# Kernel optimization log

Measured on AMD Instinct MI355X. Metric: run time of the kernel, lower is better.

The kernel has to match this reference:

```python
import jax, jax.numpy as jnp
import numpy as np

N, E, F_IN, HID, HEADS, NT, B = 50000, 400000, 32, 64, 4, 20, 64
IN1 = F_IN + HID  # 96, conv1 input dim after concat with node-type embedding


def _glorot(key, shape):
    fan_in = shape[0]
    return jax.random.normal(key, shape, dtype=jnp.float32) / np.sqrt(fan_in)


def setup_inputs() -> dict:
    key = jax.random.key(0)
    ks = jax.random.split(key, 40)
    inp = {
        "x": jax.random.normal(ks[0], (N, F_IN), dtype=jnp.float32),
        "edge_index": jax.random.randint(ks[1], (2, E), 0, N, dtype=jnp.int32),
        "edge_attr": jax.random.normal(ks[2], (E,), dtype=jnp.float32),
        "batch": jnp.sort(jax.random.randint(ks[3], (N,), 0, B, dtype=jnp.int32)),
        "node_type": jax.random.randint(ks[4], (N,), 0, NT, dtype=jnp.int32),
        # parameters
        "node_emb": jax.random.normal(ks[5], (NT, HID), dtype=jnp.float32) * 0.1,
        "edge_W": _glorot(ks[6], (1, HID)), "edge_b": jnp.zeros((HID,), jnp.float32),
        # GATConv 1 (in=96, out=64, heads=4, edge_dim=64, concat=False)
        "W1": _glorot(ks[7], (IN1, HEADS * HID)),
        "att_src1": jax.random.normal(ks[8], (HEADS, HID), jnp.float32) * 0.1,
        "att_dst1": jax.random.normal(ks[9], (HEADS, HID), jnp.float32) * 0.1,
        "We1": _glorot(ks[10], (HID, HEADS * HID)),
        "att_e1": jax.random.normal(ks[11], (HEADS, HID), jnp.float32) * 0.1,
        "b1": jnp.zeros((HID,), jnp.float32),
        # GATConv 2 (in=64)
        "W2": _glorot(ks[12], (HID, HEADS * HID)),
        "att_src2": jax.random.normal(ks[13], (HEADS, HID), jnp.float32) * 0.1,
        "att_dst2": jax.random.normal(ks[14], (HEADS, HID), jnp.float32) * 0.1,
        "We2": _glorot(ks[15], (HID, HEADS * HID)),
        "att_e2": jax.random.normal(ks[16], (HEADS, HID), jnp.float32) * 0.1,
        "b2": jnp.zeros((HID,), jnp.float32),
        # SAGEConv (mean aggr): out = mean_agg @ Wl + x @ Wr + b
        "sage_Wl": _glorot(ks[17], (HID, HID)), "sage_Wr": _glorot(ks[18], (HID, HID)),
        "sage_b": jnp.zeros((HID,), jnp.float32),
        "lin1_W": _glorot(ks[19], (HID, HID)), "lin1_b": jnp.zeros((HID,), jnp.float32),
        "lin2_W": _glorot(ks[20], (HID, HID)), "lin2_b": jnp.zeros((HID,), jnp.float32),
        "tel_W": _glorot(ks[21], (HID, 1)), "tel_b": jnp.zeros((1,), jnp.float32),
        "comp_W": _glorot(ks[22], (HID, 1)), "comp_b": jnp.zeros((1,), jnp.float32),
        "pch_W": _glorot(ks[23], (HID, 1)), "pch_b": jnp.zeros((1,), jnp.float32),
    }
    return inp


def _gat(x, src, dst, edge_h, W, att_s, att_d, We, att_e, b):
    n = x.shape[0]
    h = (x @ W).reshape(n, HEADS, HID)                       # [N,H,C]
    a_s = (h * att_s).sum(-1)                                # [N,H]
    a_d = (h * att_d).sum(-1)
    e = (edge_h @ We).reshape(-1, HEADS, HID)                # [E,H,C]
    a_e = (e * att_e).sum(-1)                                # [E,H]
    alpha = jax.nn.leaky_relu(a_s[src] + a_d[dst] + a_e, 0.2)
    m = jax.ops.segment_max(alpha, dst, num_segments=n)
    m = jnp.where(jnp.isfinite(m), m, 0.0)
    ex = jnp.exp(alpha - m[dst])
    den = jax.ops.segment_sum(ex, dst, num_segments=n)
    alpha = ex / (den[dst] + 1e-16)                          # segment softmax per dst
    out = jax.ops.segment_sum(h[src] * alpha[..., None], dst, num_segments=n)
    return out.mean(axis=1) + b                              # concat=False -> head mean


def reference(x, edge_index, edge_attr, batch, node_type, node_emb, edge_W, edge_b,
              W1, att_src1, att_dst1, We1, att_e1, b1,
              W2, att_src2, att_dst2, We2, att_e2, b2,
              sage_Wl, sage_Wr, sage_b, lin1_W, lin1_b, lin2_W, lin2_b,
              tel_W, tel_b, comp_W, comp_b, pch_W, pch_b):
    src, dst = edge_index[0], edge_index[1]
    edge_h = edge_attr[:, None] @ edge_W + edge_b            # [E,HID]
    h = jnp.concatenate([x, node_emb[node_type]], axis=-1)   # [N,96]
    h = jax.nn.elu(_gat(h, src, dst, edge_h, W1, att_src1, att_dst1, We1, att_e1, b1))
    h = jax.nn.elu(_gat(h, src, dst, edge_h, W2, att_src2, att_dst2, We2, att_e2, b2))
    # SAGEConv with mean aggregation
    deg = jax.ops.segment_sum(jnp.ones((src.shape[0],), h.dtype), dst, num_segments=N)
    agg = jax.ops.segment_sum(h[src], dst, num_segments=N) / jnp.maximum(deg, 1.0)[:, None]
    h = jax.nn.elu(agg @ sage_Wl + h @ sage_Wr + sage_b)
    # global mean pool over graphs
    cnt = jax.ops.segment_sum(jnp.ones((N,), h.dtype), batch, num_segments=B)
    g = jax.ops.segment_sum(h, batch, num_segments=B) / jnp.maximum(cnt, 1.0)[:, None]
    g = jax.nn.elu(g @ lin1_W + lin1_b)                      # dropout is identity in eval
    g = g @ lin2_W + lin2_b
    return (g @ tel_W + tel_b, g @ comp_W + comp_b, g @ pch_W + pch_b)
```

## Files before the change

### kernel.cpp

```cpp
#include <hip/hip_runtime.h>
#include <hip/hip_bf16.h>


#define NN 50000
#define NE 400000
#define FIN 32
#define NBATCH 64

typedef __hip_bfloat16 bf16;
typedef short bf16x8 __attribute__((ext_vector_type(8)));
typedef float f32x4 __attribute__((ext_vector_type(4)));

__device__ __forceinline__ float b2f(bf16 v) { return __bfloat162float(v); }
__device__ __forceinline__ float lrelu(float x) { return x > 0.f ? x : 0.2f * x; }
__device__ __forceinline__ float eluf(float x) { return x > 0.f ? x : (expf(x) - 1.f); }

__device__ __forceinline__ float4 f4fma(float s, float4 w, float4 c) {
  c.x = fmaf(s, w.x, c.x); c.y = fmaf(s, w.y, c.y);
  c.z = fmaf(s, w.z, c.z); c.w = fmaf(s, w.w, c.w);
  return c;
}

__device__ __forceinline__ float4 upk4(uint2 u) {
  float4 f;
  f.x = __uint_as_float(u.x << 16);
  f.y = __uint_as_float(u.x & 0xffff0000u);
  f.z = __uint_as_float(u.y << 16);
  f.w = __uint_as_float(u.y & 0xffff0000u);
  return f;
}

__device__ __forceinline__ unsigned short bfbits(float f) {
  bf16 b = __float2bfloat16(f);
  unsigned short u;
  __builtin_memcpy(&u, &b, 2);
  return u;
}
__device__ __forceinline__ float hi_f(unsigned short u) {
  return __uint_as_float((unsigned int)u << 16);
}

__global__ __launch_bounds__(256) void k_pq(
    const float* __restrict__ We1, const float* __restrict__ atte1,
    const float* __restrict__ We2, const float* __restrict__ atte2,
    const float* __restrict__ edgeW, const float* __restrict__ edgeB,
    float* __restrict__ pq) {
  int t = threadIdx.x, h = t >> 6, c = t & 63;
  float sW1 = 0.f, sB1 = 0.f, sW2 = 0.f, sB2 = 0.f;
  for (int j = 0; j < 64; ++j) {
    float w = edgeW[j], b = edgeB[j];
    float we1 = We1[j * 256 + h * 64 + c];
    float we2 = We2[j * 256 + h * 64 + c];
    sW1 += w * we1; sB1 += b * we1;
    sW2 += w * we2; sB2 += b * we2;
  }
  float a1 = atte1[h * 64 + c], a2 = atte2[h * 64 + c];
  float p1 = sW1 * a1, q1 = sB1 * a1, p2 = sW2 * a2, q2 = sB2 * a2;
  for (int o = 32; o; o >>= 1) {
    p1 += __shfl_xor(p1, o); q1 += __shfl_xor(q1, o);
    p2 += __shfl_xor(p2, o); q2 += __shfl_xor(q2, o);
  }
  if (c == 0) { pq[h] = p1; pq[4 + h] = q1; pq[8 + h] = p2; pq[12 + h] = q2; }
}

__global__ void k_hist(const int* __restrict__ dst, int* __restrict__ cnt) {
  int e = blockIdx.x * 256 + threadIdx.x;
  if (e < NE) atomicAdd(&cnt[dst[e]], 1);
}

__global__ __launch_bounds__(1024) void k_scan(const int* __restrict__ cnt,
                                               int* __restrict__ off) {
  __shared__ int wsum[16];
  __shared__ int carry;
  int t = threadIdx.x, lane = t & 63, w = t >> 6;
  if (t == 0) { carry = 0; off[0] = 0; }
  __syncthreads();
  for (int base = 0; base < NN; base += 1024) {
    int idx = base + t;
    int v = (idx < NN) ? cnt[idx] : 0;
    int s = v;
    for (int o = 1; o < 64; o <<= 1) { int u = __shfl_up(s, o); if (lane >= o) s += u; }
    if (lane == 63) wsum[w] = s;
    __syncthreads();
    if (t < 16) {
      int ws = wsum[t];
      for (int o = 1; o < 16; o <<= 1) { int u = __shfl_up(ws, o); if (t >= o) ws += u; }
      wsum[t] = ws;
    }
    __syncthreads();
    int add = carry + (w ? wsum[w - 1] : 0);
    if (idx < NN) off[idx + 1] = add + s;
    __syncthreads();
    if (t == 0) carry += wsum[15];
    __syncthreads();
  }
}

__global__ void k_scatter(const int* __restrict__ src, const int* __restrict__ dst,
                          const float* __restrict__ ea, const int* __restrict__ off,
                          int* __restrict__ cur, int* __restrict__ csr_src,
                          float* __restrict__ csr_ea) {
  int e = blockIdx.x * 256 + threadIdx.x;
  if (e >= NE) return;
  int d = dst[e];
  int slot = off[d] + atomicAdd(&cur[d], 1);
  csr_src[slot] = src[e];
  csr_ea[slot] = ea[e];
}

__global__ __launch_bounds__(256) void k_splitA(
    const float* __restrict__ x, const int* __restrict__ ntype,
    const float* __restrict__ emb, unsigned short* __restrict__ Ah,
    unsigned short* __restrict__ Al) {
  const int total = NN * 96;
  for (int i = blockIdx.x * 256 + threadIdx.x; i < total; i += gridDim.x * 256) {
    int n = i / 96, k = i - n * 96;
    float v = (k < FIN) ? x[n * FIN + k] : emb[ntype[n] * 64 + (k - FIN)];
    unsigned short h = bfbits(v);
    Ah[i] = h;
    Al[i] = bfbits(v - hi_f(h));
  }
}

__global__ __launch_bounds__(256) void k_splitW(
    const float* __restrict__ W1, const float* __restrict__ W2,
    unsigned short* __restrict__ B1h, unsigned short* __restrict__ B1l,
    unsigned short* __restrict__ B2h, unsigned short* __restrict__ B2l) {
  int t = blockIdx.x * 256 + threadIdx.x;
  if (t < 256 * 96) {
    int n = t / 96, k = t - n * 96;
    float v = W1[k * 256 + n];
    unsigned short h = bfbits(v);
    B1h[t] = h; B1l[t] = bfbits(v - hi_f(h));
  }
  if (t < 256 * 64) {
    int n = t >> 6, k = t & 63;
    float v = W2[k * 256 + n];
    unsigned short h = bfbits(v);
    B2h[t] = h; B2l[t] = bfbits(v - hi_f(h));
  }
}

template <int K>
__global__ __launch_bounds__(256) void k_mm_mfma(
    const unsigned short* __restrict__ Ah, const unsigned short* __restrict__ Al,
    const unsigned short* __restrict__ Bh, const unsigned short* __restrict__ Bl,
    const float* __restrict__ atts, const float* __restrict__ attd,
    bf16* __restrict__ hmat, float* __restrict__ as_, float* __restrict__ ad_) {
  int m0 = blockIdx.x * 64;
  int w = threadIdx.x >> 6;
  int lane = threadIdx.x & 63;
  int lr = lane & 15;
  int lc = lane >> 4;
  float attsv[4], attdv[4];
  #pragma unroll
  for (int nt = 0; nt < 4; ++nt) {
    attsv[nt] = atts[w * 64 + nt * 16 + lr];
    attdv[nt] = attd[w * 64 + nt * 16 + lr];
  }
  f32x4 acc[4][4] = {};
  #pragma unroll
  for (int ks = 0; ks < K; ks += 32) {
    int koff = ks + lc * 8;
    bf16x8 ah[4], al[4], bh[4], bl[4];
    #pragma unroll
    for (int mt = 0; mt < 4; ++mt) {
      int m = m0 + mt * 16 + lr;
      if (m > NN - 1) m = NN - 1;
      ah[mt] = *reinterpret_cast<const bf16x8*>(&Ah[(size_t)m * K + koff]);
      al[mt] = *reinterpret_cast<const bf16x8*>(&Al[(size_t)m * K + koff]);
    }
    #pragma unroll
    for (int nt = 0; nt < 4; ++nt) {
      int n = w * 64 + nt * 16 + lr;
      bh[nt] = *reinterpret_cast<const bf16x8*>(&Bh[(size_t)n * K + koff]);
      bl[nt] = *reinterpret_cast<const bf16x8*>(&Bl[(size_t)n * K + koff]);
    }
    #pragma unroll
    for (int mt = 0; mt < 4; ++mt) {
      #pragma unroll
      for (int nt = 0; nt < 4; ++nt) {
        acc[mt][nt] = __builtin_amdgcn_mfma_f32_16x16x32_bf16(ah[mt], bh[nt], acc[mt][nt], 0, 0, 0);
        acc[mt][nt] = __builtin_amdgcn_mfma_f32_16x16x32_bf16(al[mt], bh[nt], acc[mt][nt], 0, 0, 0);
        acc[mt][nt] = __builtin_amdgcn_mfma_f32_16x16x32_bf16(ah[mt], bl[nt], acc[mt][nt], 0, 0, 0);
      }
    }
  }
  #pragma unroll
  for (int mt = 0; mt < 4; ++mt) {
    #pragma unroll
    for (int reg = 0; reg < 4; ++reg) {
      int row = m0 + mt * 16 + lc * 4 + reg;
      float sS = 0.f, sD = 0.f;
      #pragma unroll
      for (int nt = 0; nt < 4; ++nt) {
        float v = acc[mt][nt][reg];
        sS += v * attsv[nt];
        sD += v * attdv[nt];
      }
      for (int o = 1; o < 16; o <<= 1) {
        sS += __shfl_xor(sS, o);
        sD += __shfl_xor(sD, o);
      }
      if (row < NN) {
        #pragma unroll
        for (int nt = 0; nt < 4; ++nt)
          hmat[(size_t)row * 256 + w * 64 + nt * 16 + lr] =
              __float2bfloat16(acc[mt][nt][reg]);
        if (lr == 0) { as_[row * 4 + w] = sS; ad_[row * 4 + w] = sD; }
      }
    }
  }
}

__global__ __launch_bounds__(256) void k_gat(
    const int* __restrict__ off, const int* __restrict__ csr_src,
    const float* __restrict__ csr_ea, const float* __restrict__ as_,
    const float* __restrict__ ad_, const float* __restrict__ pq, int pqo,
    const bf16* __restrict__ hmat, const float* __restrict__ bias,
    float* __restrict__ outf, unsigned short* __restrict__ oph,
    unsigned short* __restrict__ opl) {
  __shared__ float wlds[4][256];
  int wv = threadIdx.x >> 6;
  int wid = (blockIdx.x << 2) + wv;
  int lane = threadIdx.x & 63;
  if (wid >= NN) return;
  int beg = off[wid], end = off[wid + 1];
  int deg = end - beg;
  int hsel = lane >> 4;
  float4 D = reinterpret_cast<const float4*>(ad_)[wid];
  float p0 = pq[pqo + 0], p1 = pq[pqo + 1], p2 = pq[pqo + 2], p3 = pq[pqo + 3];
  float q0 = pq[pqo + 4], q1 = pq[pqo + 5], q2 = pq[pqo + 6], q3 = pq[pqo + 7];
  float4 acc = {0.f, 0.f, 0.f, 0.f};

  if (deg <= 64) {
    bool valid = lane < deg;
    float lx = -INFINITY, ly = -INFINITY, lz = -INFINITY, lw = -INFINITY;
    if (valid) {
      int s = csr_src[beg + lane];
      float ea = csr_ea[beg + lane];
      float4 A = reinterpret_cast<const float4*>(as_)[s];
      lx = lrelu(A.x + D.x + ea * p0 + q0);
      ly = lrelu(A.y + D.y + ea * p1 + q1);
      lz = lrelu(A.z + D.z + ea * p2 + q2);
      lw = lrelu(A.w + D.w + ea * p3 + q3);
    }
    float m0 = lx, m1 = ly, m2 = lz, m3 = lw;
    for (int o = 32; o; o >>= 1) {
      m0 = fmaxf(m0, __shfl_xor(m0, o));
      m1 = fmaxf(m1, __shfl_xor(m1, o));
      m2 = fmaxf(m2, __shfl_xor(m2, o));
      m3 = fmaxf(m3, __shfl_xor(m3, o));
    }
    float w0 = valid ? __expf(lx - m0) : 0.f;
    float w1 = valid ? __expf(ly - m1) : 0.f;
    float w2 = valid ? __expf(lz - m2) : 0.f;
    float w3 = valid ? __expf(lw - m3) : 0.f;
    float s0 = w0, s1 = w1, s2 = w2, s3 = w3;
    for (int o = 32; o; o >>= 1) {
      s0 += __shfl_xor(s0, o); s1 += __shfl_xor(s1, o);
      s2 += __shfl_xor(s2, o); s3 += __shfl_xor(s3, o);
    }
    float4 wv4;
    wv4.x = w0 / (s0 + 1e-16f);
    wv4.y = w1 / (s1 + 1e-16f);
    wv4.z = w2 / (s2 + 1e-16f);
    wv4.w = w3 / (s3 + 1e-16f);
    reinterpret_cast<float4*>(&wlds[wv][0])[lane] = wv4;
    const float* wp = &wlds[wv][0];
    int j = 0;
    for (; j + 4 <= deg; j += 4) {
      int sA = csr_src[beg + j + 0];
      int sB = csr_src[beg + j + 1];
      int sC = csr_src[beg + j + 2];
      int sD = csr_src[beg + j + 3];
      float wA = wp[4 * (j + 0) + hsel];
      float wB = wp[4 * (j + 1) + hsel];
      float wC = wp[4 * (j + 2) + hsel];
      float wD = wp[4 * (j + 3) + hsel];
      uint2 uA = *reinterpret_cast<const uint2*>(&hmat[(size_t)sA * 256 + 4 * lane]);
      uint2 uB = *reinterpret_cast<const uint2*>(&hmat[(size_t)sB * 256 + 4 * lane]);
      uint2 uC = *reinterpret_cast<const uint2*>(&hmat[(size_t)sC * 256 + 4 * lane]);
      uint2 uD = *reinterpret_cast<const uint2*>(&hmat[(size_t)sD * 256 + 4 * lane]);
      acc = f4fma(wA, upk4(uA), acc);
      acc = f4fma(wB, upk4(uB), acc);
      acc = f4fma(wC, upk4(uC), acc);
      acc = f4fma(wD, upk4(uD), acc);
    }
    for (; j < deg; ++j) {
      int s = csr_src[beg + j];
      float w = wp[4 * j + hsel];
      uint2 u = *reinterpret_cast<const uint2*>(&hmat[(size_t)s * 256 + 4 * lane]);
      acc = f4fma(w, upk4(u), acc);
    }
  } else {
    float m0 = -INFINITY, m1 = -INFINITY, m2 = -INFINITY, m3 = -INFINITY;
    float s0 = 0.f, s1 = 0.f, s2 = 0.f, s3 = 0.f;
    for (int e = beg + lane; e < end; e += 64) {
      int s = csr_src[e];
      float ea = csr_ea[e];
      float4 A = reinterpret_cast<const float4*>(as_)[s];
      float lx = lrelu(A.x + D.x + ea * p0 + q0);
      float ly = lrelu(A.y + D.y + ea * p1 + q1);
      float lz = lrelu(A.z + D.z + ea * p2 + q2);
      float lw = lrelu(A.w + D.w + ea * p3 + q3);
      float nm;
      nm = fmaxf(m0, lx); s0 = s0 * __expf(m0 - nm) + __expf(lx - nm); m0 = nm;
      nm = fmaxf(m1, ly); s1 = s1 * __expf(m1 - nm) + __expf(ly - nm); m1 = nm;
      nm = fmaxf(m2, lz); s2 = s2 * __expf(m2 - nm) + __expf(lz - nm); m2 = nm;
      nm = fmaxf(m3, lw); s3 = s3 * __expf(m3 - nm) + __expf(lw - nm); m3 = nm;
    }
    for (int o = 32; o; o >>= 1) {
      float om, os, nm;
      om = __shfl_xor(m0, o); os = __shfl_xor(s0, o); nm = fmaxf(m0, om);
      s0 = s0 * __expf(fmaxf(m0 - nm, -80.f)) + os * __expf(fmaxf(om - nm, -80.f)); m0 = nm;
      om = __shfl_xor(m1, o); os = __shfl_xor(s1, o); nm = fmaxf(m1, om);
      s1 = s1 * __expf(fmaxf(m1 - nm, -80.f)) + os * __expf(fmaxf(om - nm, -80.f)); m1 = nm;
      om = __shfl_xor(m2, o); os = __shfl_xor(s2, o); nm = fmaxf(m2, om);
      s2 = s2 * __expf(fmaxf(m2 - nm, -80.f)) + os * __expf(fmaxf(om - nm, -80.f)); m2 = nm;
      om = __shfl_xor(m3, o); os = __shfl_xor(s3, o); nm = fmaxf(m3, om);
      s3 = s3 * __expf(fmaxf(m3 - nm, -80.f)) + os * __expf(fmaxf(om - nm, -80.f)); m3 = nm;
    }
    float i0 = 1.f / (s0 + 1e-16f), i1 = 1.f / (s1 + 1e-16f);
    float i2 = 1.f / (s2 + 1e-16f), i3 = 1.f / (s3 + 1e-16f);
    float Dh = hsel == 0 ? D.x : hsel == 1 ? D.y : hsel == 2 ? D.z : D.w;
    float ph = hsel == 0 ? p0 : hsel == 1 ? p1 : hsel == 2 ? p2 : p3;
    float qh = hsel == 0 ? q0 : hsel == 1 ? q1 : hsel == 2 ? q2 : q3;
    float mh = hsel == 0 ? m0 : hsel == 1 ? m1 : hsel == 2 ? m2 : m3;
    float ih = hsel == 0 ? i0 : hsel == 1 ? i1 : hsel == 2 ? i2 : i3;
    for (int j = beg; j < end; ++j) {
      int s = csr_src[j];
      float ea = csr_ea[j];
      float4 A = reinterpret_cast<const float4*>(as_)[s];
      float Ah = hsel == 0 ? A.x : hsel == 1 ? A.y : hsel == 2 ? A.z : A.w;
      float l = lrelu(Ah + Dh + ea * ph + qh);
      float w = __expf(l - mh) * ih;
      uint2 u = *reinterpret_cast<const uint2*>(&hmat[(size_t)s * 256 + 4 * lane]);
      acc = f4fma(w, upk4(u), acc);
    }
  }
  acc.x += __shfl_xor(acc.x, 16); acc.y += __shfl_xor(acc.y, 16);
  acc.z += __shfl_xor(acc.z, 16); acc.w += __shfl_xor(acc.w, 16);
  acc.x += __shfl_xor(acc.x, 32); acc.y += __shfl_xor(acc.y, 32);
  acc.z += __shfl_xor(acc.z, 32); acc.w += __shfl_xor(acc.w, 32);
  if (lane < 16) {
    float4 bv = reinterpret_cast<const float4*>(bias)[lane];
    float4 r;
    r.x = eluf(0.25f * acc.x + bv.x);
    r.y = eluf(0.25f * acc.y + bv.y);
    r.z = eluf(0.25f * acc.z + bv.z);
    r.w = eluf(0.25f * acc.w + bv.w);
    if (outf) reinterpret_cast<float4*>(&outf[(size_t)wid * 64])[lane] = r;
    if (oph) {
      ushort4 h4, l4;
      h4.x = bfbits(r.x); l4.x = bfbits(r.x - hi_f(h4.x));
      h4.y = bfbits(r.y); l4.y = bfbits(r.y - hi_f(h4.y));
      h4.z = bfbits(r.z); l4.z = bfbits(r.z - hi_f(h4.z));
      h4.w = bfbits(r.w); l4.w = bfbits(r.w - hi_f(h4.w));
      *reinterpret_cast<ushort4*>(&oph[(size_t)wid * 64 + lane * 4]) = h4;
      *reinterpret_cast<ushort4*>(&opl[(size_t)wid * 64 + lane * 4]) = l4;
    }
  }
}

__global__ __launch_bounds__(256) void k_agg(
    const int* __restrict__ off, const int* __restrict__ csr_src,
    const float* __restrict__ h3, float* __restrict__ agg) {
  int wid = (blockIdx.x << 2) + (threadIdx.x >> 6);
  int lane = threadIdx.x & 63;
  if (wid >= NN) return;
  int beg = off[wid], end = off[wid + 1];
  float acc = 0.f;
  int e = beg;
  for (; e + 4 <= end; e += 4) {
    int s0 = csr_src[e + 0], s1 = csr_src[e + 1];
    int s2 = csr_src[e + 2], s3 = csr_src[e + 3];
    float v0 = h3[(size_t)s0 * 64 + lane];
    float v1 = h3[(size_t)s1 * 64 + lane];
    float v2 = h3[(size_t)s2 * 64 + lane];
    float v3 = h3[(size_t)s3 * 64 + lane];
    acc += (v0 + v1) + (v2 + v3);
  }
  for (; e < end; ++e) acc += h3[(size_t)csr_src[e] * 64 + lane];
  agg[(size_t)wid * 64 + lane] = acc / fmaxf((float)(end - beg), 1.f);
}

__global__ __launch_bounds__(256) void k_sage_mm(
    const float* __restrict__ agg, const float* __restrict__ h3,
    const float* __restrict__ Wl, const float* __restrict__ Wr,
    const float* __restrict__ bias, float* __restrict__ out) {
  __shared__ float WlS[4096];
  __shared__ float WrS[4096];
  __shared__ float Ag[2048];
  __shared__ float Hr[2048];
  int t = threadIdx.x;
  for (int i = t; i < 4096; i += 256) { WlS[i] = Wl[i]; WrS[i] = Wr[i]; }
  int ct = t & 15, rg = t >> 4;
  float4 bv = reinterpret_cast<const float4*>(bias)[ct];
  for (int r0 = blockIdx.x * 32; r0 < NN; r0 += gridDim.x * 32) {
    for (int i = t; i < 2048; i += 256) {
      int n = r0 + (i >> 6);
      float va = 0.f, vh = 0.f;
      if (n < NN) {
        va = agg[(size_t)n * 64 + (i & 63)];
        vh = h3[(size_t)n * 64 + (i & 63)];
      }
      Ag[i] = va; Hr[i] = vh;
    }
    __syncthreads();
    float4 c0 = {0.f, 0.f, 0.f, 0.f}, c1 = c0;
    const float* a0 = &Ag[(rg * 2 + 0) * 64];
    const float* a1 = &Ag[(rg * 2 + 1) * 64];
    const float* h0 = &Hr[(rg * 2 + 0) * 64];
    const float* h1 = &Hr[(rg * 2 + 1) * 64];
    #pragma unroll 4
    for (int k = 0; k < 64; k += 4) {
      float4 wl0 = *reinterpret_cast<const float4*>(&WlS[(k + 0) * 64 + ct * 4]);
      float4 wl1 = *reinterpret_cast<const float4*>(&WlS[(k + 1) * 64 + ct * 4]);
      float4 wl2 = *reinterpret_cast<const float4*>(&WlS[(k + 2) * 64 + ct * 4]);
      float4 wl3 = *reinterpret_cast<const float4*>(&WlS[(k + 3) * 64 + ct * 4]);
      float4 wr0 = *reinterpret_cast<const float4*>(&WrS[(k + 0) * 64 + ct * 4]);
      float4 wr1 = *reinterpret_cast<const float4*>(&WrS[(k + 1) * 64 + ct * 4]);
      float4 wr2 = *reinterpret_cast<const float4*>(&WrS[(k + 2) * 64 + ct * 4]);
      float4 wr3 = *reinterpret_cast<const float4*>(&WrS[(k + 3) * 64 + ct * 4]);
      float4 aa0 = *reinterpret_cast<const float4*>(&a0[k]);
      float4 aa1 = *reinterpret_cast<const float4*>(&a1[k]);
      float4 hh0 = *reinterpret_cast<const float4*>(&h0[k]);
      float4 hh1 = *reinterpret_cast<const float4*>(&h1[k]);
      c0 = f4fma(aa0.x, wl0, c0); c0 = f4fma(aa0.y, wl1, c0);
      c0 = f4fma(aa0.z, wl2, c0); c0 = f4fma(aa0.w, wl3, c0);
      c0 = f4fma(hh0.x, wr0, c0); c0 = f4fma(hh0.y, wr1, c0);
      c0 = f4fma(hh0.z, wr2, c0); c0 = f4fma(hh0.w, wr3, c0);
      c1 = f4fma(aa1.x, wl0, c1); c1 = f4fma(aa1.y, wl1, c1);
      c1 = f4fma(aa1.z, wl2, c1); c1 = f4fma(aa1.w, wl3, c1);
      c1 = f4fma(hh1.x, wr0, c1); c1 = f4fma(hh1.y, wr1, c1);
      c1 = f4fma(hh1.z, wr2, c1); c1 = f4fma(hh1.w, wr3, c1);
    }
    int n0 = r0 + rg * 2;
    if (n0 + 0 < NN) {
      float4 r;
      r.x = eluf(c0.x + bv.x); r.y = eluf(c0.y + bv.y);
      r.z = eluf(c0.z + bv.z); r.w = eluf(c0.w + bv.w);
      *reinterpret_cast<float4*>(&out[(size_t)(n0 + 0) * 64 + ct * 4]) = r;
    }
    if (n0 + 1 < NN) {
      float4 r;
      r.x = eluf(c1.x + bv.x); r.y = eluf(c1.y + bv.y);
      r.z = eluf(c1.z + bv.z); r.w = eluf(c1.w + bv.w);
      *reinterpret_cast<float4*>(&out[(size_t)(n0 + 1) * 64 + ct * 4]) = r;
    }
    __syncthreads();
  }
}

__global__ __launch_bounds__(256) void k_pool2(const float* __restrict__ hs,
                                               const int* __restrict__ batch,
                                               float* __restrict__ g) {
  int cid = (blockIdx.x << 2) + (threadIdx.x >> 6);
  int lane = threadIdx.x & 63;
  int n0 = cid * 32;
  if (n0 >= NN) return;
  int n1 = n0 + 32 < NN ? n0 + 32 : NN;
  int cur = batch[n0];
  float acc = 0.f;
  for (int n = n0; n < n1; ++n) {
    int b = batch[n];
    if (b != cur) {
      atomicAdd(&g[cur * 64 + lane], acc);
      acc = 0.f;
      cur = b;
    }
    acc += hs[(size_t)n * 64 + lane];
  }
  atomicAdd(&g[cur * 64 + lane], acc);
}

__device__ __forceinline__ int lowerb(const int* __restrict__ a, int n, int key) {
  int lo = 0, hi = n;
  while (lo < hi) { int mid = (lo + hi) >> 1; if (a[mid] < key) lo = mid + 1; else hi = mid; }
  return lo;
}

__global__ __launch_bounds__(256) void k_head(
    const float* __restrict__ g, const int* __restrict__ batch,
    const float* __restrict__ l1W, const float* __restrict__ l1b,
    const float* __restrict__ l2W, const float* __restrict__ l2b,
    const float* __restrict__ telW, const float* __restrict__ telb,
    const float* __restrict__ compW, const float* __restrict__ compb,
    const float* __restrict__ pchW, const float* __restrict__ pchb,
    float* __restrict__ out) {
  __shared__ float gS[4096];
  __shared__ float WS[4096];
  __shared__ float hS[4096];
  __shared__ float invc[64];
  int t = threadIdx.x;
  if (t < 64) {
    int lo = lowerb(batch, NN, t), hi = lowerb(batch, NN, t + 1);
    invc[t] = 1.f / fmaxf((float)(hi - lo), 1.f);
  }
  for (int i = t; i < 4096; i += 256) WS[i] = l1W[i];
  __syncthreads();
  for (int i = t; i < 4096; i += 256) gS[i] = g[i] * invc[i >> 6];
  __syncthreads();
  for (int i = t; i < 4096; i += 256) {
    int r = i >> 6, j = i & 63;
    float s = 0.f;
    for (int k = 0; k < 64; ++k) s += gS[r * 64 + k] * WS[k * 64 + j];
    hS[i] = eluf(s + l1b[j]);
  }
  __syncthreads();
  for (int i = t; i < 4096; i += 256) WS[i] = l2W[i];
  __syncthreads();
  for (int i = t; i < 4096; i += 256) {
    int r = i >> 6, j = i & 63;
    float s = 0.f;
    for (int k = 0; k < 64; ++k) s += hS[r * 64 + k] * WS[k * 64 + j];
    gS[i] = s + l2b[j];
  }
  __syncthreads();
  if (t < 192) {
    int head = t >> 6, r = t & 63;
    const float* Wv = head == 0 ? telW : (head == 1 ? compW : pchW);
    float bb = head == 0 ? telb[0] : (head == 1 ? compb[0] : pchb[0]);
    float s = 0.f;
    for (int k = 0; k < 64; ++k) s += gS[r * 64 + k] * Wv[k];
    out[t] = s + bb;
  }
}

extern "C" void kernel_launch(void* const* d_in, const int* in_sizes, int n_in,
                              void* d_out, int out_size, void* d_ws, size_t ws_size,
                              hipStream_t stream) {
  const float* x     = (const float*)d_in[0];
  const int*   eidx  = (const int*)d_in[1];
  const float* eattr = (const float*)d_in[2];
  const int*   batch = (const int*)d_in[3];
  const int*   ntype = (const int*)d_in[4];
  const float* nemb  = (const float*)d_in[5];
  const float* edgeW = (const float*)d_in[6];
  const float* edgeB = (const float*)d_in[7];
  const float* W1    = (const float*)d_in[8];
  const float* atts1 = (const float*)d_in[9];
  const float* attd1 = (const float*)d_in[10];
  const float* We1   = (const float*)d_in[11];
  const float* atte1 = (const float*)d_in[12];
  const float* b1    = (const float*)d_in[13];
  const float* W2    = (const float*)d_in[14];
  const float* atts2 = (const float*)d_in[15];
  const float* attd2 = (const float*)d_in[16];
  const float* We2   = (const float*)d_in[17];
  const float* atte2 = (const float*)d_in[18];
  const float* b2    = (const float*)d_in[19];
  const float* sageWl = (const float*)d_in[20];
  const float* sageWr = (const float*)d_in[21];
  const float* sageB  = (const float*)d_in[22];
  const float* l1W = (const float*)d_in[23];
  const float* l1b = (const float*)d_in[24];
  const float* l2W = (const float*)d_in[25];
  const float* l2b = (const float*)d_in[26];
  const float* telW  = (const float*)d_in[27];
  const float* telb  = (const float*)d_in[28];
  const float* compW = (const float*)d_in[29];
  const float* compb = (const float*)d_in[30];
  const float* pchW  = (const float*)d_in[31];
  const float* pchb  = (const float*)d_in[32];

  char* wp = (char*)d_ws;
  auto alloc = [&](size_t bytes) -> char* {
    char* p = wp;
    wp += (bytes + 255) & ~(size_t)255;
    return p;
  };
  float*  pq      = (float*)alloc(16 * 4);
  int*    cnt     = (int*)alloc((size_t)NN * 4);
  int*    off     = (int*)alloc(((size_t)NN + 1) * 4);
  int*    csr_src = (int*)alloc((size_t)NE * 4);
  float*  csr_ea  = (float*)alloc((size_t)NE * 4);
  float*  as_     = (float*)alloc((size_t)NN * 16);
  float*  ad_     = (float*)alloc((size_t)NN * 16);
  bf16*   hmat    = (bf16*)alloc((size_t)NN * 256 * 2);
  float*  nodeB   = (float*)alloc((size_t)NN * 64 * 4);
  float*  aggbuf  = (float*)alloc((size_t)NN * 64 * 4);
  unsigned short* B1h = (unsigned short*)alloc(256 * 96 * 2);
  unsigned short* B1l = (unsigned short*)alloc(256 * 96 * 2);
  unsigned short* B2h = (unsigned short*)alloc(256 * 64 * 2);
  unsigned short* B2l = (unsigned short*)alloc(256 * 64 * 2);
  char* R = alloc((size_t)NN * 96 * 2 * 2);
  unsigned short* A1h = (unsigned short*)R;
  unsigned short* A1l = A1h + (size_t)NN * 96;
  unsigned short* A2h = (unsigned short*)R;
  unsigned short* A2l = A2h + (size_t)NN * 64;
  float* sageout = (float*)R;
  float* gbuf = (float*)alloc(64 * 64 * 4);

  const int* srcI = eidx;
  const int* dstI = eidx + NE;

  hipMemsetAsync(cnt, 0, (size_t)NN * 4, stream);
  hipMemsetAsync(gbuf, 0, 64 * 64 * 4, stream);
  k_pq<<<1, 256, 0, stream>>>(We1, atte1, We2, atte2, edgeW, edgeB, pq);
  k_hist<<<(NE + 255) / 256, 256, 0, stream>>>(dstI, cnt);
  k_scan<<<1, 1024, 0, stream>>>(cnt, off);
  hipMemsetAsync(cnt, 0, (size_t)NN * 4, stream);
  k_scatter<<<(NE + 255) / 256, 256, 0, stream>>>(srcI, dstI, eattr, off, cnt,
                                                  csr_src, csr_ea);
  k_splitW<<<96, 256, 0, stream>>>(W1, W2, B1h, B1l, B2h, B2l);
  k_splitA<<<2048, 256, 0, stream>>>(x, ntype, nemb, A1h, A1l);
  k_mm_mfma<96><<<(NN + 63) / 64, 256, 0, stream>>>(
      A1h, A1l, B1h, B1l, atts1, attd1, hmat, as_, ad_);
  k_gat<<<NN / 4, 256, 0, stream>>>(off, csr_src, csr_ea, as_, ad_, pq, 0,
                                    hmat, b1, nullptr, A2h, A2l);
  k_mm_mfma<64><<<(NN + 63) / 64, 256, 0, stream>>>(
      A2h, A2l, B2h, B2l, atts2, attd2, hmat, as_, ad_);
  k_gat<<<NN / 4, 256, 0, stream>>>(off, csr_src, csr_ea, as_, ad_, pq, 8,
                                    hmat, b2, nodeB, nullptr, nullptr);
  k_agg<<<NN / 4, 256, 0, stream>>>(off, csr_src, nodeB, aggbuf);
  k_sage_mm<<<1024, 256, 0, stream>>>(aggbuf, nodeB, sageWl, sageWr, sageB,
                                      sageout);
  k_pool2<<<((NN + 31) / 32 + 3) / 4, 256, 0, stream>>>(sageout, batch, gbuf);
  k_head<<<1, 256, 0, stream>>>(gbuf, batch, l1W, l1b, l2W, l2b, telW, telb,
                                compW, compb, pchW, pchb, (float*)d_out);
}
```

Before: 468.2 us.

## Widen GAT/SAGE gathers to 128-bit loads with multi-edge lanes; merge prep kernels

In the low-degree GAT path, each half-wave now gathers a different neighbor row using 16-byte loads, with 8 features per lane, and the halves are then reduced with cross-lane shuffles. The SAGE mean-aggregation kernel likewise has four lane groups each loading a different neighbor's row as float4, reduced with shuffles at the end. The weight-split kernel is merged into the pq kernel, and the scatter now counts down the histogram with atomicSub, which removes a memset. These changes aim to raise memory-level parallelism, cut load instructions and drop launches, at the cost of extra shuffle reductions and lanes idling on ragged tails.

```diff
diff --git a/kernel.cpp b/kernel.cpp
--- a/kernel.cpp
+++ b/kernel.cpp
@@ -30,6 +30,15 @@
   return f;
 }
 
+__device__ __forceinline__ float4 upk4u(unsigned int lo, unsigned int hi) {
+  float4 f;
+  f.x = __uint_as_float(lo << 16);
+  f.y = __uint_as_float(lo & 0xffff0000u);
+  f.z = __uint_as_float(hi << 16);
+  f.w = __uint_as_float(hi & 0xffff0000u);
+  return f;
+}
+
 __device__ __forceinline__ unsigned short bfbits(float f) {
   bf16 b = __float2bfloat16(f);
   unsigned short u;
@@ -40,27 +49,46 @@
   return __uint_as_float((unsigned int)u << 16);
 }
 
-__global__ __launch_bounds__(256) void k_pq(
+__global__ __launch_bounds__(256) void k_prep(
+    const float* __restrict__ W1, const float* __restrict__ W2,
     const float* __restrict__ We1, const float* __restrict__ atte1,
     const float* __restrict__ We2, const float* __restrict__ atte2,
     const float* __restrict__ edgeW, const float* __restrict__ edgeB,
+    unsigned short* __restrict__ B1h, unsigned short* __restrict__ B1l,
+    unsigned short* __restrict__ B2h, unsigned short* __restrict__ B2l,
     float* __restrict__ pq) {
-  int t = threadIdx.x, h = t >> 6, c = t & 63;
-  float sW1 = 0.f, sB1 = 0.f, sW2 = 0.f, sB2 = 0.f;
-  for (int j = 0; j < 64; ++j) {
-    float w = edgeW[j], b = edgeB[j];
-    float we1 = We1[j * 256 + h * 64 + c];
-    float we2 = We2[j * 256 + h * 64 + c];
-    sW1 += w * we1; sB1 += b * we1;
-    sW2 += w * we2; sB2 += b * we2;
-  }
-  float a1 = atte1[h * 64 + c], a2 = atte2[h * 64 + c];
-  float p1 = sW1 * a1, q1 = sB1 * a1, p2 = sW2 * a2, q2 = sB2 * a2;
-  for (int o = 32; o; o >>= 1) {
-    p1 += __shfl_xor(p1, o); q1 += __shfl_xor(q1, o);
-    p2 += __shfl_xor(p2, o); q2 += __shfl_xor(q2, o);
-  }
-  if (c == 0) { pq[h] = p1; pq[4 + h] = q1; pq[8 + h] = p2; pq[12 + h] = q2; }
+  if (blockIdx.x == 96) {
+    int t = threadIdx.x, h = t >> 6, c = t & 63;
+    float sW1 = 0.f, sB1 = 0.f, sW2 = 0.f, sB2 = 0.f;
+    for (int j = 0; j < 64; ++j) {
+      float w = edgeW[j], b = edgeB[j];
+      float we1 = We1[j * 256 + h * 64 + c];
+      float we2 = We2[j * 256 + h * 64 + c];
+      sW1 += w * we1; sB1 += b * we1;
+      sW2 += w * we2; sB2 += b * we2;
+    }
+    float a1 = atte1[h * 64 + c], a2 = atte2[h * 64 + c];
+    float p1 = sW1 * a1, q1 = sB1 * a1, p2 = sW2 * a2, q2 = sB2 * a2;
+    for (int o = 32; o; o >>= 1) {
+      p1 += __shfl_xor(p1, o); q1 += __shfl_xor(q1, o);
+      p2 += __shfl_xor(p2, o); q2 += __shfl_xor(q2, o);
+    }
+    if (c == 0) { pq[h] = p1; pq[4 + h] = q1; pq[8 + h] = p2; pq[12 + h] = q2; }
+    return;
+  }
+  int t = blockIdx.x * 256 + threadIdx.x;
+  if (t < 256 * 96) {
+    int n = t / 96, k = t - n * 96;
+    float v = W1[k * 256 + n];
+    unsigned short h = bfbits(v);
+    B1h[t] = h; B1l[t] = bfbits(v - hi_f(h));
+  }
+  if (t < 256 * 64) {
+    int n = t >> 6, k = t & 63;
+    float v = W2[k * 256 + n];
+    unsigned short h = bfbits(v);
+    B2h[t] = h; B2l[t] = bfbits(v - hi_f(h));
+  }
 }
 
 __global__ void k_hist(const int* __restrict__ dst, int* __restrict__ cnt) {
@@ -98,12 +126,13 @@
 
 __global__ void k_scatter(const int* __restrict__ src, const int* __restrict__ dst,
                           const float* __restrict__ ea, const int* __restrict__ off,
-                          int* __restrict__ cur, int* __restrict__ csr_src,
+                          int* __restrict__ cnt, int* __restrict__ csr_src,
                           float* __restrict__ csr_ea) {
   int e = blockIdx.x * 256 + threadIdx.x;
   if (e >= NE) return;
   int d = dst[e];
-  int slot = off[d] + atomicAdd(&cur[d], 1);
+  int r = atomicSub(&cnt[d], 1);
+  int slot = off[d] + r - 1;
   csr_src[slot] = src[e];
   csr_ea[slot] = ea[e];
 }
@@ -119,25 +148,6 @@
     unsigned short h = bfbits(v);
     Ah[i] = h;
     Al[i] = bfbits(v - hi_f(h));
-  }
-}
-
-__global__ __launch_bounds__(256) void k_splitW(
-    const float* __restrict__ W1, const float* __restrict__ W2,
-    unsigned short* __restrict__ B1h, unsigned short* __restrict__ B1l,
-    unsigned short* __restrict__ B2h, unsigned short* __restrict__ B2l) {
-  int t = blockIdx.x * 256 + threadIdx.x;
-  if (t < 256 * 96) {
-    int n = t / 96, k = t - n * 96;
-    float v = W1[k * 256 + n];
-    unsigned short h = bfbits(v);
-    B1h[t] = h; B1l[t] = bfbits(v - hi_f(h));
-  }
-  if (t < 256 * 64) {
-    int n = t >> 6, k = t & 63;
-    float v = W2[k * 256 + n];
-    unsigned short h = bfbits(v);
-    B2h[t] = h; B2l[t] = bfbits(v - hi_f(h));
   }
 }
 
@@ -227,11 +237,9 @@
   if (wid >= NN) return;
   int beg = off[wid], end = off[wid + 1];
   int deg = end - beg;
-  int hsel = lane >> 4;
   float4 D = reinterpret_cast<const float4*>(ad_)[wid];
   float p0 = pq[pqo + 0], p1 = pq[pqo + 1], p2 = pq[pqo + 2], p3 = pq[pqo + 3];
   float q0 = pq[pqo + 4], q1 = pq[pqo + 5], q2 = pq[pqo + 6], q3 = pq[pqo + 7];
-  float4 acc = {0.f, 0.f, 0.f, 0.f};
 
   if (deg <= 64) {
     bool valid = lane < deg;
@@ -268,32 +276,71 @@
     wv4.w = w3 / (s3 + 1e-16f);
     reinterpret_cast<float4*>(&wlds[wv][0])[lane] = wv4;
     const float* wp = &wlds[wv][0];
+    int g = lane >> 5;
+    int c5 = lane & 31;
+    int hsl = c5 >> 3;
+    float4 aA = {0.f, 0.f, 0.f, 0.f}, aB = aA;
     int j = 0;
-    for (; j + 4 <= deg; j += 4) {
-      int sA = csr_src[beg + j + 0];
-      int sB = csr_src[beg + j + 1];
-      int sC = csr_src[beg + j + 2];
-      int sD = csr_src[beg + j + 3];
-      float wA = wp[4 * (j + 0) + hsel];
-      float wB = wp[4 * (j + 1) + hsel];
-      float wC = wp[4 * (j + 2) + hsel];
-      float wD = wp[4 * (j + 3) + hsel];
-      uint2 uA = *reinterpret_cast<const uint2*>(&hmat[(size_t)sA * 256 + 4 * lane]);
-      uint2 uB = *reinterpret_cast<const uint2*>(&hmat[(size_t)sB * 256 + 4 * lane]);
-      uint2 uC = *reinterpret_cast<const uint2*>(&hmat[(size_t)sC * 256 + 4 * lane]);
-      uint2 uD = *reinterpret_cast<const uint2*>(&hmat[(size_t)sD * 256 + 4 * lane]);
-      acc = f4fma(wA, upk4(uA), acc);
-      acc = f4fma(wB, upk4(uB), acc);
-      acc = f4fma(wC, upk4(uC), acc);
-      acc = f4fma(wD, upk4(uD), acc);
-    }
-    for (; j < deg; ++j) {
-      int s = csr_src[beg + j];
-      float w = wp[4 * j + hsel];
-      uint2 u = *reinterpret_cast<const uint2*>(&hmat[(size_t)s * 256 + 4 * lane]);
-      acc = f4fma(w, upk4(u), acc);
+    for (; j + 8 <= deg; j += 8) {
+      #pragma unroll
+      for (int p = 0; p < 4; ++p) {
+        int jj = j + 2 * p;
+        int sA = csr_src[beg + jj];
+        int sB = csr_src[beg + jj + 1];
+        int s = g ? sB : sA;
+        float w = wp[4 * (jj + g) + hsl];
+        uint4 u = *reinterpret_cast<const uint4*>(&hmat[(size_t)s * 256 + c5 * 8]);
+        aA = f4fma(w, upk4u(u.x, u.y), aA);
+        aB = f4fma(w, upk4u(u.z, u.w), aB);
+      }
+    }
+    for (; j < deg; j += 2) {
+      int sA = csr_src[beg + j];
+      int sB = (j + 1 < deg) ? csr_src[beg + j + 1] : sA;
+      bool act = (j + g) < deg;
+      int s = g ? sB : sA;
+      float w = act ? wp[4 * (j + g) + hsl] : 0.f;
+      uint4 u = *reinterpret_cast<const uint4*>(&hmat[(size_t)s * 256 + c5 * 8]);
+      aA = f4fma(w, upk4u(u.x, u.y), aA);
+      aB = f4fma(w, upk4u(u.z, u.w), aB);
+    }
+    #pragma unroll
+    for (int o = 8; o <= 32; o <<= 1) {
+      aA.x += __shfl_xor(aA.x, o); aA.y += __shfl_xor(aA.y, o);
+      aA.z += __shfl_xor(aA.z, o); aA.w += __shfl_xor(aA.w, o);
+      aB.x += __shfl_xor(aB.x, o); aB.y += __shfl_xor(aB.y, o);
+      aB.z += __shfl_xor(aB.z, o); aB.w += __shfl_xor(aB.w, o);
+    }
+    if (lane < 8) {
+      float4 b0 = *reinterpret_cast<const float4*>(&bias[lane * 8]);
+      float4 b1v = *reinterpret_cast<const float4*>(&bias[lane * 8 + 4]);
+      float4 rA, rB;
+      rA.x = eluf(0.25f * aA.x + b0.x);  rA.y = eluf(0.25f * aA.y + b0.y);
+      rA.z = eluf(0.25f * aA.z + b0.z);  rA.w = eluf(0.25f * aA.w + b0.w);
+      rB.x = eluf(0.25f * aB.x + b1v.x); rB.y = eluf(0.25f * aB.y + b1v.y);
+      rB.z = eluf(0.25f * aB.z + b1v.z); rB.w = eluf(0.25f * aB.w + b1v.w);
+      if (outf) {
+        float4* o = reinterpret_cast<float4*>(&outf[(size_t)wid * 64 + lane * 8]);
+        o[0] = rA; o[1] = rB;
+      }
+      if (oph) {
+        ushort4 h4, l4;
+        h4.x = bfbits(rA.x); l4.x = bfbits(rA.x - hi_f(h4.x));
+        h4.y = bfbits(rA.y); l4.y = bfbits(rA.y - hi_f(h4.y));
+        h4.z = bfbits(rA.z); l4.z = bfbits(rA.z - hi_f(h4.z));
+        h4.w = bfbits(rA.w); l4.w = bfbits(rA.w - hi_f(h4.w));
+        *reinterpret_cast<ushort4*>(&oph[(size_t)wid * 64 + lane * 8]) = h4;
+        *reinterpret_cast<ushort4*>(&opl[(size_t)wid * 64 + lane * 8]) = l4;
+        h4.x = bfbits(rB.x); l4.x = bfbits(rB.x - hi_f(h4.x));
+        h4.y = bfbits(rB.y); l4.y = bfbits(rB.y - hi_f(h4.y));
+        h4.z = bfbits(rB.z); l4.z = bfbits(rB.z - hi_f(h4.z));
+        h4.w = bfbits(rB.w); l4.w = bfbits(rB.w - hi_f(h4.w));
+        *reinterpret_cast<ushort4*>(&oph[(size_t)wid * 64 + lane * 8 + 4]) = h4;
+        *reinterpret_cast<ushort4*>(&opl[(size_t)wid * 64 + lane * 8 + 4]) = l4;
+      }
     }
   } else {
+    int hsel = lane >> 4;
     float m0 = -INFINITY, m1 = -INFINITY, m2 = -INFINITY, m3 = -INFINITY;
     float s0 = 0.f, s1 = 0.f, s2 = 0.f, s3 = 0.f;
     for (int e = beg + lane; e < end; e += 64) {
@@ -328,6 +375,7 @@
     float qh = hsel == 0 ? q0 : hsel == 1 ? q1 : hsel == 2 ? q2 : q3;
     float mh = hsel == 0 ? m0 : hsel == 1 ? m1 : hsel == 2 ? m2 : m3;
     float ih = hsel == 0 ? i0 : hsel == 1 ? i1 : hsel == 2 ? i2 : i3;
+    float4 acc = {0.f, 0.f, 0.f, 0.f};
     for (int j = beg; j < end; ++j) {
       int s = csr_src[j];
       float ea = csr_ea[j];
@@ -338,27 +386,27 @@
       uint2 u = *reinterpret_cast<const uint2*>(&hmat[(size_t)s * 256 + 4 * lane]);
       acc = f4fma(w, upk4(u), acc);
     }
-  }
-  acc.x += __shfl_xor(acc.x, 16); acc.y += __shfl_xor(acc.y, 16);
-  acc.z += __shfl_xor(acc.z, 16); acc.w += __shfl_xor(acc.w, 16);
-  acc.x += __shfl_xor(acc.x, 32); acc.y += __shfl_xor(acc.y, 32);
-  acc.z += __shfl_xor(acc.z, 32); acc.w += __shfl_xor(acc.w, 32);
-  if (lane < 16) {
-    float4 bv = reinterpret_cast<const float4*>(bias)[lane];
-    float4 r;
-    r.x = eluf(0.25f * acc.x + bv.x);
-    r.y = eluf(0.25f * acc.y + bv.y);
-    r.z = eluf(0.25f * acc.z + bv.z);
-    r.w = eluf(0.25f * acc.w + bv.w);
-    if (outf) reinterpret_cast<float4*>(&outf[(size_t)wid * 64])[lane] = r;
-    if (oph) {
-      ushort4 h4, l4;
-      h4.x = bfbits(r.x); l4.x = bfbits(r.x - hi_f(h4.x));
-      h4.y = bfbits(r.y); l4.y = bfbits(r.y - hi_f(h4.y));
-      h4.z = bfbits(r.z); l4.z = bfbits(r.z - hi_f(h4.z));
-      h4.w = bfbits(r.w); l4.w = bfbits(r.w - hi_f(h4.w));
-      *reinterpret_cast<ushort4*>(&oph[(size_t)wid * 64 + lane * 4]) = h4;
-      *reinterpret_cast<ushort4*>(&opl[(size_t)wid * 64 + lane * 4]) = l4;
+    acc.x += __shfl_xor(acc.x, 16); acc.y += __shfl_xor(acc.y, 16);
+    acc.z += __shfl_xor(acc.z, 16); acc.w += __shfl_xor(acc.w, 16);
+    acc.x += __shfl_xor(acc.x, 32); acc.y += __shfl_xor(acc.y, 32);
+    acc.z += __shfl_xor(acc.z, 32); acc.w += __shfl_xor(acc.w, 32);
+    if (lane < 16) {
+      float4 bv = reinterpret_cast<const float4*>(bias)[lane];
+      float4 r;
+      r.x = eluf(0.25f * acc.x + bv.x);
+      r.y = eluf(0.25f * acc.y + bv.y);
+      r.z = eluf(0.25f * acc.z + bv.z);
+      r.w = eluf(0.25f * acc.w + bv.w);
+      if (outf) reinterpret_cast<float4*>(&outf[(size_t)wid * 64])[lane] = r;
+      if (oph) {
+        ushort4 h4, l4;
+        h4.x = bfbits(r.x); l4.x = bfbits(r.x - hi_f(h4.x));
+        h4.y = bfbits(r.y); l4.y = bfbits(r.y - hi_f(h4.y));
+        h4.z = bfbits(r.z); l4.z = bfbits(r.z - hi_f(h4.z));
+        h4.w = bfbits(r.w); l4.w = bfbits(r.w - hi_f(h4.w));
+        *reinterpret_cast<ushort4*>(&oph[(size_t)wid * 64 + lane * 4]) = h4;
+        *reinterpret_cast<ushort4*>(&opl[(size_t)wid * 64 + lane * 4]) = l4;
+      }
     }
   }
 }
@@ -370,19 +418,45 @@
   int lane = threadIdx.x & 63;
   if (wid >= NN) return;
   int beg = off[wid], end = off[wid + 1];
-  float acc = 0.f;
-  int e = beg;
-  for (; e + 4 <= end; e += 4) {
-    int s0 = csr_src[e + 0], s1 = csr_src[e + 1];
-    int s2 = csr_src[e + 2], s3 = csr_src[e + 3];
-    float v0 = h3[(size_t)s0 * 64 + lane];
-    float v1 = h3[(size_t)s1 * 64 + lane];
-    float v2 = h3[(size_t)s2 * 64 + lane];
-    float v3 = h3[(size_t)s3 * 64 + lane];
-    acc += (v0 + v1) + (v2 + v3);
-  }
-  for (; e < end; ++e) acc += h3[(size_t)csr_src[e] * 64 + lane];
-  agg[(size_t)wid * 64 + lane] = acc / fmaxf((float)(end - beg), 1.f);
+  int deg = end - beg;
+  int g = lane >> 4;
+  int c4 = lane & 15;
+  float4 acc = {0.f, 0.f, 0.f, 0.f};
+  int j = 0;
+  for (; j + 8 <= deg; j += 8) {
+    #pragma unroll
+    for (int p = 0; p < 2; ++p) {
+      int jj = j + 4 * p;
+      int s0 = csr_src[beg + jj + 0];
+      int s1 = csr_src[beg + jj + 1];
+      int s2 = csr_src[beg + jj + 2];
+      int s3 = csr_src[beg + jj + 3];
+      int s = g < 2 ? (g == 0 ? s0 : s1) : (g == 2 ? s2 : s3);
+      float4 v = *reinterpret_cast<const float4*>(&h3[(size_t)s * 64 + c4 * 4]);
+      acc.x += v.x; acc.y += v.y; acc.z += v.z; acc.w += v.w;
+    }
+  }
+  for (; j < deg; j += 4) {
+    int lim = deg - j;
+    int s0 = csr_src[beg + j];
+    int s1 = (lim > 1) ? csr_src[beg + j + 1] : s0;
+    int s2 = (lim > 2) ? csr_src[beg + j + 2] : s0;
+    int s3 = (lim > 3) ? csr_src[beg + j + 3] : s0;
+    int s = g < 2 ? (g == 0 ? s0 : s1) : (g == 2 ? s2 : s3);
+    float4 v = *reinterpret_cast<const float4*>(&h3[(size_t)s * 64 + c4 * 4]);
+    if (g < lim) { acc.x += v.x; acc.y += v.y; acc.z += v.z; acc.w += v.w; }
+  }
+  #pragma unroll
+  for (int o = 16; o <= 32; o <<= 1) {
+    acc.x += __shfl_xor(acc.x, o); acc.y += __shfl_xor(acc.y, o);
+    acc.z += __shfl_xor(acc.z, o); acc.w += __shfl_xor(acc.w, o);
+  }
+  if (lane < 16) {
+    float inv = 1.f / fmaxf((float)deg, 1.f);
+    float4 r;
+    r.x = acc.x * inv; r.y = acc.y * inv; r.z = acc.z * inv; r.w = acc.w * inv;
+    reinterpret_cast<float4*>(&agg[(size_t)wid * 64])[c4] = r;
+  }
 }
 
 __global__ __launch_bounds__(256) void k_sage_mm(
@@ -598,13 +672,12 @@
 
   hipMemsetAsync(cnt, 0, (size_t)NN * 4, stream);
   hipMemsetAsync(gbuf, 0, 64 * 64 * 4, stream);
-  k_pq<<<1, 256, 0, stream>>>(We1, atte1, We2, atte2, edgeW, edgeB, pq);
+  k_prep<<<97, 256, 0, stream>>>(W1, W2, We1, atte1, We2, atte2, edgeW, edgeB,
+                                 B1h, B1l, B2h, B2l, pq);
   k_hist<<<(NE + 255) / 256, 256, 0, stream>>>(dstI, cnt);
   k_scan<<<1, 1024, 0, stream>>>(cnt, off);
-  hipMemsetAsync(cnt, 0, (size_t)NN * 4, stream);
   k_scatter<<<(NE + 255) / 256, 256, 0, stream>>>(srcI, dstI, eattr, off, cnt,
                                                   csr_src, csr_ea);
-  k_splitW<<<96, 256, 0, stream>>>(W1, W2, B1h, B1l, B2h, B2l);
   k_splitA<<<2048, 256, 0, stream>>>(x, ntype, nemb, A1h, A1l);
   k_mm_mfma<96><<<(NN + 63) / 64, 256, 0, stream>>>(
       A1h, A1l, B1h, B1l, atts1, attd1, hmat, as_, ad_);
```

Result: no change. 475.6 us (+1.6%).
